# Kernel tuning notes

Hardware: AMD Instinct MI355X
Metric: run time of the kernel (lower is better)

## Reference

```python
import jax, jax.numpy as jnp
from jax import lax
import numpy as np

N_NODES = 512
BATCH = 256
N_STEPS = 200
DT = 0.02  # t_span spacing; keeps 200 RK4 steps numerically tame


def setup_inputs() -> dict:
    key = jax.random.key(0)
    ks = jax.random.split(key, 7)
    s = 1.0 / np.sqrt(N_NODES)
    x_init = jax.random.normal(ks[0], (BATCH, N_NODES), dtype=jnp.float32)
    t_span = jnp.arange(N_STEPS, dtype=jnp.float32) * DT
    # MaskedLinear params (kaiming-uniform-ish scale)
    W1 = jax.random.uniform(ks[1], (N_NODES, N_NODES), jnp.float32, -s, s)
    b1 = jax.random.uniform(ks[2], (N_NODES,), jnp.float32, -s, s)
    # inner Linear params
    W2 = jax.random.uniform(ks[3], (N_NODES, N_NODES), jnp.float32, -s, s)
    b2 = jax.random.uniform(ks[4], (N_NODES,), jnp.float32, -s, s)
    mask = jax.random.bernoulli(ks[5], 0.1, (N_NODES, N_NODES)).astype(jnp.float32)
    mask = mask * (1.0 - jnp.eye(N_NODES, dtype=jnp.float32))
    return {"x_init": x_init, "t_span": t_span, "W1": W1, "b1": b1,
            "W2": W2, "b2": b2, "mask": mask}


def reference(x_init, t_span, W1, b1, W2, b2, mask):
    # ODE func: dydt = W2 @ tanh(masked(W1) @ y + b1) + b2 (t unused)
    Wm = W1 * mask  # [N, N]
    def f(y):  # y: [B, N]
        return jnp.tanh(y @ Wm.T + b1) @ W2.T + b2

    dts = t_span[1:] - t_span[:-1]  # [T-1]

    def rk4_step(y, dt):
        k1 = f(y)
        k2 = f(y + dt * k1 / 2)
        k3 = f(y + dt * k2 / 2)
        k4 = f(y + dt * k3)
        y_new = y + dt / 6 * (k1 + 2 * k2 + 2 * k3 + k4)
        return y_new, y_new

    _, traj = lax.scan(rk4_step, x_init, dts)  # [T-1, B, N]
    traj = jnp.concatenate([x_init[None], traj], axis=0)  # [T, B, N]
    return jnp.transpose(traj, (1, 0, 2))  # [B, T, N]
```

## Files before the change

kernel.cpp:

```cpp
#include <hip/hip_runtime.h>
#include <math.h>

#define NN 512
#define NB 256
#define NT 200
#define TPB 256
#define NTEAM 8

typedef unsigned long long u64;
typedef _Float16 half8 __attribute__((ext_vector_type(8)));
typedef float f32x4 __attribute__((ext_vector_type(4)));

#define WS_WM  0
#define WS_WC  (NN*NN)
#define WS_C   (WS_WC + NN*NN/2)
#define WS_H   (WS_C + NN)
#define WS_CNT (WS_H + NB*NN)

__device__ __forceinline__ void sysst_u64(u64* p, u64 v) {
  __hip_atomic_store(p, v, __ATOMIC_RELAXED, __HIP_MEMORY_SCOPE_SYSTEM);
}
__device__ __forceinline__ u64 sysld_u64(const u64* p) {
  return __hip_atomic_load(p, __ATOMIC_RELAXED, __HIP_MEMORY_SCOPE_SYSTEM);
}
__device__ __forceinline__ void sysst_f1(float* p, float v) {
  __hip_atomic_store(p, v, __ATOMIC_RELAXED, __HIP_MEMORY_SCOPE_SYSTEM);
}
__device__ __forceinline__ float sysld_f1(const float* p) {
  return __hip_atomic_load(p, __ATOMIC_RELAXED, __HIP_MEMORY_SCOPE_SYSTEM);
}

__global__ __launch_bounds__(256)
void k_init(const float* __restrict__ W1, const float* __restrict__ mask,
            const float* __restrict__ x_init, float* __restrict__ ws,
            float* __restrict__ out) {
  int gt = blockIdx.x * 256 + threadIdx.x;
  int stride = gridDim.x * 256;
  for (int i = gt; i < NN * NN; i += stride) ws[WS_WM + i] = W1[i] * mask[i];
  for (int i = gt; i < NB * NN / 2; i += stride) {
    u64 q = ((const u64*)x_init)[i];
    int r = i >> 8, np = i & 255;
    *((u64*)(out + (size_t)r * NT * NN) + np) = q;
  }
  if (gt < 32 * NTEAM * 16)
    __hip_atomic_store(((unsigned*)(ws + WS_CNT)) + gt, 0u,
                       __ATOMIC_RELAXED, __HIP_MEMORY_SCOPE_SYSTEM);
}

__global__ __launch_bounds__(128)
void k_prep(const float* __restrict__ W2g, const float* __restrict__ b2,
            const float* __restrict__ x_init, float* __restrict__ ws) {
  __shared__ float w1row[NN];
  const int j = blockIdx.x;
  const int t = threadIdx.x;
  const float* wm = ws + WS_WM + (size_t)j * NN;
  for (int i = t; i < NN; i += 128) w1row[i] = wm[i];
  __syncthreads();

  f32x4 acc = {0.f, 0.f, 0.f, 0.f};
  for (int m = 0; m < NN; ++m) {
    float w = w1row[m];
    if (w != 0.f)
      acc += w * ((const f32x4*)(W2g + (size_t)m * NN))[t];
  }
  _Float16* wcrow = (_Float16*)(ws + WS_WC) + (size_t)j * NN;
#pragma unroll
  for (int e = 0; e < 4; ++e) wcrow[4 * t + e] = (_Float16)acc[e];

  if (t == 0) {
    float s = 0.f;
    for (int m = 0; m < NN; ++m)
      if (w1row[m] != 0.f) s += b2[m] * w1row[m];
    ws[WS_C + j] = s;
  }

#pragma unroll
  for (int rr = 0; rr < 2; ++rr) {
    int r = t + rr * 128;
    const float* y0 = x_init + (size_t)r * NN;
    float s = 0.f;
    for (int m = 0; m < NN; ++m) {
      float w = w1row[m];
      if (w != 0.f) s = fmaf(y0[m], w, s);
    }
    sysst_f1(ws + WS_H + (size_t)r * NN + j, s);
  }
}

__device__ __forceinline__ void team_release(unsigned* flags, int cg, unsigned e) {
  __syncthreads();
  if (threadIdx.x == 0)
    __hip_atomic_store(flags + cg * 16, e, __ATOMIC_RELAXED,
                       __HIP_MEMORY_SCOPE_SYSTEM);
}
__device__ __forceinline__ void team_wait(unsigned* flags, unsigned e) {
  if (threadIdx.x < NTEAM) {
    while (__hip_atomic_load(flags + threadIdx.x * 16, __ATOMIC_RELAXED,
                             __HIP_MEMORY_SCOPE_AGENT) < e)
      __builtin_amdgcn_s_sleep(1);
  }
  __syncthreads();
}

__device__ __forceinline__ void stage8(_Float16* __restrict__ pH,
                                       _Float16* __restrict__ pL,
                                       const float* __restrict__ src,
                                       int tid) {
  const int row = tid >> 5;
  const int segq = tid & 31;
  const u64* s = (const u64*)(src + (size_t)row * NN) + segq * 8;
  u64 tmp[8];
#pragma unroll
  for (int i = 0; i < 8; ++i) tmp[i] = sysld_u64(s + i);
  half8* dH = (half8*)pH;
  half8* dL = (half8*)pL;
#pragma unroll
  for (int q = 0; q < 2; ++q) {
    half8 hv, lv;
#pragma unroll
    for (int e = 0; e < 4; ++e) {
      union { u64 q64; float f[2]; } u; u.q64 = tmp[q * 4 + e];
#pragma unroll
      for (int x = 0; x < 2; ++x) {
        float f = u.f[x]; _Float16 h = (_Float16)f;
        hv[e * 2 + x] = h;
        lv[e * 2 + x] = (_Float16)((f - (float)h) * 2048.0f);
      }
    }
    int g = segq * 2 + q;
    int idx = row * 64 + (g ^ row);
    dH[idx] = hv; dL[idx] = lv;
  }
}

__device__ __forceinline__ void gemm_tile(const _Float16* yHb, const _Float16* yLb,
                                          const _Float16* wb,
                                          int rc, int kg, int wv, float res[4]) {
  const int swz = rc & 7;
  const half8* pAH = (const half8*)yHb;
  const half8* pAL = (const half8*)yLb;
  const half8* pB  = (const half8*)wb;
  const int abase = (rc & 7) * 64;
  const int bbase = (wv * 16 + rc) * 64;
  f32x4 aH = {0.f, 0.f, 0.f, 0.f};
  f32x4 aL = {0.f, 0.f, 0.f, 0.f};
#pragma unroll
  for (int kt = 0; kt < 16; ++kt) {
    const int gs = (kt * 4 + kg) ^ swz;
    half8 av = pAH[abase + gs];
    half8 al = pAL[abase + gs];
    half8 bv = pB[bbase + gs];
    aH = __builtin_amdgcn_mfma_f32_16x16x32_f16(av, bv, aH, 0, 0, 0);
    aL = __builtin_amdgcn_mfma_f32_16x16x32_f16(al, bv, aL, 0, 0, 0);
  }
#pragma unroll
  for (int r = 0; r < 4; ++r) res[r] = aH[r] + aL[r] * (1.0f / 2048.0f);
}

__global__ __launch_bounds__(TPB, 1)
void k_ode(const float* __restrict__ tspan,
           const float* __restrict__ W2g,
           const float* __restrict__ b1,
           const float* __restrict__ b2,
           float* __restrict__ ws,
           float* __restrict__ out,
           const float* __restrict__ x_init) {
  extern __shared__ _Float16 ldsh[];
  _Float16* wc = ldsh;
  _Float16* w2 = ldsh + 32768;
  _Float16* hH = ldsh + 65536;
  _Float16* hL = ldsh + 73728;

  const int bid = blockIdx.x;
  const int cg = bid & 7, rg = bid >> 3;
  const int r0 = rg * 8, j0 = cg * 64;
  const int tid = threadIdx.x;
  const int lane = tid & 63, wv = tid >> 6;
  const int rc = lane & 15, kg = lane >> 4;
  const int mycol = j0 + wv * 16 + rc;
  const bool act = (kg < 2);

  float* hbuf = ws + WS_H;
  unsigned* flags = ((unsigned*)(ws + WS_CNT)) + rg * (NTEAM * 16);

  {
    const int col = tid >> 2;
    const int part = tid & 3;
    const half8* s1 = (const half8*)((const _Float16*)(ws + WS_WC)
                                     + (size_t)(j0 + col) * NN) + part * 16;
    const float* s2 = W2g + (size_t)(j0 + col) * NN + part * 128;
    half8* d1 = (half8*)wc;
    half8* d2 = (half8*)w2;
    const int key = col & 7;
#pragma unroll
    for (int i = 0; i < 16; ++i) {
      int g = part * 16 + i;
      int idx = col * 64 + (g ^ key);
      d1[idx] = s1[i];
      half8 hv;
#pragma unroll
      for (int e = 0; e < 8; ++e) hv[e] = (_Float16)s2[i * 8 + e];
      d2[idx] = hv;
    }
  }
  const float b1s = b1[mycol], b2s = b2[mycol];
  const float c_own = ws[WS_C + mycol];

  float xb[4], yb[4];
  if (act) {
#pragma unroll
    for (int r = 0; r < 4; ++r) {
      xb[r] = sysld_f1(hbuf + (size_t)(r0 + kg * 4 + r) * NN + mycol);
      yb[r] = x_init[(size_t)(r0 + kg * 4 + r) * NN + mycol];
    }
  }
  __syncthreads();

  unsigned epoch = 0;
  float res[4], res2[4];

  for (int t = 0; t < NT - 1; ++t) {
    const float dt = tspan[t + 1] - tspan[t];
    const float alf[3] = {dt * 0.5f, dt * 0.5f, dt};
    float xs[4], H[4];
    if (act) {
#pragma unroll
      for (int r = 0; r < 4; ++r) xs[r] = xb[r];
    }
#pragma unroll
    for (int s = 0; s < 3; ++s) {
      if (act) {
#pragma unroll
        for (int r = 0; r < 4; ++r) {
          float h = tanhf(xs[r] + b1s);
          H[r] = (s == 0) ? h : fmaf(2.f, h, H[r]);
          sysst_f1(hbuf + (size_t)(r0 + kg * 4 + r) * NN + mycol, h);
        }
      }
      team_release(flags, cg, ++epoch);
      team_wait(flags, epoch);
      stage8(hH, hL, hbuf + (size_t)r0 * NN, tid);
      __syncthreads();
      gemm_tile(hH, hL, wc, rc, kg, wv, res);
      if (act) {
#pragma unroll
        for (int r = 0; r < 4; ++r)
          xs[r] = xb[r] + alf[s] * (res[r] + c_own);
      }
    }
    if (act) {
#pragma unroll
      for (int r = 0; r < 4; ++r) {
        H[r] += tanhf(xs[r] + b1s);
        sysst_f1(hbuf + (size_t)(r0 + kg * 4 + r) * NN + mycol, H[r]);
      }
    }
    team_release(flags, cg, ++epoch);
    team_wait(flags, epoch);
    stage8(hH, hL, hbuf + (size_t)r0 * NN, tid);
    __syncthreads();
    gemm_tile(hH, hL, wc, rc, kg, wv, res);
    gemm_tile(hH, hL, w2, rc, kg, wv, res2);
    if (act) {
      const float c6 = dt / 6.0f;
#pragma unroll
      for (int r = 0; r < 4; ++r) {
        xb[r] += c6 * res[r] + dt * c_own;
        yb[r] += c6 * res2[r] + dt * b2s;
        out[((size_t)(r0 + kg * 4 + r) * NT + (t + 1)) * NN + mycol] = yb[r];
      }
    }
  }
}

extern "C" void kernel_launch(void* const* d_in, const int* in_sizes, int n_in,
                              void* d_out, int out_size, void* d_ws, size_t ws_size,
                              hipStream_t stream) {
  const float* x_init = (const float*)d_in[0];
  const float* tspan  = (const float*)d_in[1];
  const float* W1     = (const float*)d_in[2];
  const float* b1     = (const float*)d_in[3];
  const float* W2     = (const float*)d_in[4];
  const float* b2     = (const float*)d_in[5];
  const float* mask   = (const float*)d_in[6];
  float* out = (float*)d_out;
  float* ws  = (float*)d_ws;

  hipLaunchKernelGGL(k_init, dim3(256), dim3(256), 0, stream,
                     W1, mask, x_init, ws, out);
  hipLaunchKernelGGL(k_prep, dim3(512), dim3(128), 0, stream,
                     W2, b2, x_init, ws);

  const unsigned ldsBytes = 160 * 1024;
  (void)hipFuncSetAttribute((const void*)k_ode,
                            hipFuncAttributeMaxDynamicSharedMemorySize,
                            (int)ldsBytes);

  hipLaunchKernelGGL(k_ode, dim3(256), dim3(TPB), ldsBytes, stream,
                     tspan, W2, b1, b2, ws, out, x_init);
}
```

Before: 2.895 ms.

## Split team sync into two half-row groups with double-buffered hidden state

Result: slower. 3.666 ms (+26.6%).

```diff
diff --git a/kernel.cpp b/kernel.cpp
--- a/kernel.cpp
+++ b/kernel.cpp
@@ -42,7 +42,7 @@
     int r = i >> 8, np = i & 255;
     *((u64*)(out + (size_t)r * NT * NN) + np) = q;
   }
-  if (gt < 32 * NTEAM * 16)
+  if (gt < 32 * 2 * NTEAM * 16)
     __hip_atomic_store(((unsigned*)(ws + WS_CNT)) + gt, 0u,
                        __ATOMIC_RELAXED, __HIP_MEMORY_SCOPE_SYSTEM);
 }
@@ -87,50 +87,46 @@
   }
 }
 
-__device__ __forceinline__ void team_release(unsigned* flags, int cg, unsigned e) {
+__device__ __forceinline__ void team_wait(unsigned* flagsp, unsigned target) {
+  if (threadIdx.x < NTEAM) {
+    while (__hip_atomic_load(flagsp + threadIdx.x * 16, __ATOMIC_RELAXED,
+                             __HIP_MEMORY_SCOPE_AGENT) < target)
+      __builtin_amdgcn_s_sleep(1);
+  }
+  __syncthreads();
+}
+__device__ __forceinline__ void team_release(unsigned* flagsp, int cg, unsigned e) {
   __syncthreads();
   if (threadIdx.x == 0)
-    __hip_atomic_store(flags + cg * 16, e, __ATOMIC_RELAXED,
+    __hip_atomic_store(flagsp + cg * 16, e, __ATOMIC_RELAXED,
                        __HIP_MEMORY_SCOPE_SYSTEM);
 }
-__device__ __forceinline__ void team_wait(unsigned* flags, unsigned e) {
-  if (threadIdx.x < NTEAM) {
-    while (__hip_atomic_load(flags + threadIdx.x * 16, __ATOMIC_RELAXED,
-                             __HIP_MEMORY_SCOPE_AGENT) < e)
-      __builtin_amdgcn_s_sleep(1);
-  }
-  __syncthreads();
-}
-
-__device__ __forceinline__ void stage8(_Float16* __restrict__ pH,
+
+__device__ __forceinline__ void stage4(_Float16* __restrict__ pH,
                                        _Float16* __restrict__ pL,
                                        const float* __restrict__ src,
-                                       int tid) {
-  const int row = tid >> 5;
-  const int segq = tid & 31;
-  const u64* s = (const u64*)(src + (size_t)row * NN) + segq * 8;
-  u64 tmp[8];
-#pragma unroll
-  for (int i = 0; i < 8; ++i) tmp[i] = sysld_u64(s + i);
-  half8* dH = (half8*)pH;
-  half8* dL = (half8*)pL;
-#pragma unroll
-  for (int q = 0; q < 2; ++q) {
-    half8 hv, lv;
-#pragma unroll
-    for (int e = 0; e < 4; ++e) {
-      union { u64 q64; float f[2]; } u; u.q64 = tmp[q * 4 + e];
-#pragma unroll
-      for (int x = 0; x < 2; ++x) {
-        float f = u.f[x]; _Float16 h = (_Float16)f;
-        hv[e * 2 + x] = h;
-        lv[e * 2 + x] = (_Float16)((f - (float)h) * 2048.0f);
-      }
-    }
-    int g = segq * 2 + q;
-    int idx = row * 64 + (g ^ row);
-    dH[idx] = hv; dL[idx] = lv;
-  }
+                                       int p, int tid) {
+  const int row = tid >> 6;
+  const int g = tid & 63;
+  const u64* s = (const u64*)(src + (size_t)row * NN) + g * 4;
+  u64 tmp[4];
+#pragma unroll
+  for (int i = 0; i < 4; ++i) tmp[i] = sysld_u64(s + i);
+  half8 hv, lv;
+#pragma unroll
+  for (int e = 0; e < 4; ++e) {
+    union { u64 q64; float f[2]; } u; u.q64 = tmp[e];
+#pragma unroll
+    for (int x = 0; x < 2; ++x) {
+      float f = u.f[x]; _Float16 h = (_Float16)f;
+      hv[e * 2 + x] = h;
+      lv[e * 2 + x] = (_Float16)((f - (float)h) * 2048.0f);
+    }
+  }
+  const int dr = p * 4 + row;
+  const int idx = dr * 64 + (g ^ dr);
+  ((half8*)pH)[idx] = hv;
+  ((half8*)pL)[idx] = lv;
 }
 
 __device__ __forceinline__ void gemm_tile(const _Float16* yHb, const _Float16* yLb,
@@ -169,7 +165,7 @@
   _Float16* wc = ldsh;
   _Float16* w2 = ldsh + 32768;
   _Float16* hH = ldsh + 65536;
-  _Float16* hL = ldsh + 73728;
+  _Float16* hL = ldsh + 69632;
 
   const int bid = blockIdx.x;
   const int cg = bid & 7, rg = bid >> 3;
@@ -180,8 +176,11 @@
   const int mycol = j0 + wv * 16 + rc;
   const bool act = (kg < 2);
 
-  float* hbuf = ws + WS_H;
-  unsigned* flags = ((unsigned*)(ws + WS_CNT)) + rg * (NTEAM * 16);
+  float* hb[2];
+  hb[0] = ws + WS_H;
+  hb[1] = ws + WS_WM;
+  unsigned* flagsA = ((unsigned*)(ws + WS_CNT)) + rg * (2 * NTEAM * 16);
+  unsigned* flagsB = flagsA + NTEAM * 16;
 
   {
     const int col = tid >> 2;
@@ -206,68 +205,68 @@
   const float b1s = b1[mycol], b2s = b2[mycol];
   const float c_own = ws[WS_C + mycol];
 
-  float xb[4], yb[4];
+  float xb[4], yb[4], H[4];
   if (act) {
 #pragma unroll
     for (int r = 0; r < 4; ++r) {
-      xb[r] = sysld_f1(hbuf + (size_t)(r0 + kg * 4 + r) * NN + mycol);
+      xb[r] = sysld_f1(hb[0] + (size_t)(r0 + kg * 4 + r) * NN + mycol);
       yb[r] = x_init[(size_t)(r0 + kg * 4 + r) * NN + mycol];
+      H[r] = tanhf(xb[r] + b1s);
+      sysst_f1(hb[0] + (size_t)(r0 + kg * 4 + r) * NN + mycol, H[r]);
     }
   }
   __syncthreads();
-
-  unsigned epoch = 0;
+  if (tid == 0) {
+    __hip_atomic_store(flagsA + cg * 16, 1u, __ATOMIC_RELAXED,
+                       __HIP_MEMORY_SCOPE_SYSTEM);
+    __hip_atomic_store(flagsB + cg * 16, 1u, __ATOMIC_RELAXED,
+                       __HIP_MEMORY_SCOPE_SYSTEM);
+  }
+
   float res[4], res2[4];
 
   for (int t = 0; t < NT - 1; ++t) {
     const float dt = tspan[t + 1] - tspan[t];
-    const float alf[3] = {dt * 0.5f, dt * 0.5f, dt};
-    float xs[4], H[4];
-    if (act) {
-#pragma unroll
-      for (int r = 0; r < 4; ++r) xs[r] = xb[r];
-    }
-#pragma unroll
-    for (int s = 0; s < 3; ++s) {
-      if (act) {
-#pragma unroll
-        for (int r = 0; r < 4; ++r) {
-          float h = tanhf(xs[r] + b1s);
-          H[r] = (s == 0) ? h : fmaf(2.f, h, H[r]);
-          sysst_f1(hbuf + (size_t)(r0 + kg * 4 + r) * NN + mycol, h);
+    const float c6 = dt / 6.0f;
+#pragma unroll 1
+    for (int s = 0; s < 4; ++s) {
+      const int q = t * 4 + s;
+      const unsigned target = (unsigned)(q + 1);
+      const float* rdb = hb[q & 1];
+      float* wrb = hb[(q + 1) & 1];
+#pragma unroll
+      for (int p = 0; p < 2; ++p) {
+        unsigned* fl = p ? flagsB : flagsA;
+        team_wait(fl, target);
+        stage4(hH, hL, rdb + (size_t)(r0 + p * 4) * NN, p, tid);
+        __syncthreads();
+        gemm_tile(hH, hL, wc, rc, kg, wv, res);
+        if (s == 3) gemm_tile(hH, hL, w2, rc, kg, wv, res2);
+        if (kg == p) {
+          if (s < 3) {
+            const float a = (s == 2) ? dt : dt * 0.5f;
+#pragma unroll
+            for (int r = 0; r < 4; ++r) {
+              float xs = xb[r] + a * (res[r] + c_own);
+              float h = tanhf(xs + b1s);
+              float st;
+              if (s == 2) { H[r] += h;       st = H[r]; }
+              else        { H[r] += 2.f * h; st = h;    }
+              sysst_f1(wrb + (size_t)(r0 + p * 4 + r) * NN + mycol, st);
+            }
+          } else {
+#pragma unroll
+            for (int r = 0; r < 4; ++r) {
+              xb[r] += c6 * res[r] + dt * c_own;
+              yb[r] += c6 * res2[r] + dt * b2s;
+              out[((size_t)(r0 + p * 4 + r) * NT + (t + 1)) * NN + mycol] = yb[r];
+              float h = tanhf(xb[r] + b1s);
+              H[r] = h;
+              sysst_f1(wrb + (size_t)(r0 + p * 4 + r) * NN + mycol, h);
+            }
+          }
         }
-      }
-      team_release(flags, cg, ++epoch);
-      team_wait(flags, epoch);
-      stage8(hH, hL, hbuf + (size_t)r0 * NN, tid);
-      __syncthreads();
-      gemm_tile(hH, hL, wc, rc, kg, wv, res);
-      if (act) {
-#pragma unroll
-        for (int r = 0; r < 4; ++r)
-          xs[r] = xb[r] + alf[s] * (res[r] + c_own);
-      }
-    }
-    if (act) {
-#pragma unroll
-      for (int r = 0; r < 4; ++r) {
-        H[r] += tanhf(xs[r] + b1s);
-        sysst_f1(hbuf + (size_t)(r0 + kg * 4 + r) * NN + mycol, H[r]);
-      }
-    }
-    team_release(flags, cg, ++epoch);
-    team_wait(flags, epoch);
-    stage8(hH, hL, hbuf + (size_t)r0 * NN, tid);
-    __syncthreads();
-    gemm_tile(hH, hL, wc, rc, kg, wv, res);
-    gemm_tile(hH, hL, w2, rc, kg, wv, res2);
-    if (act) {
-      const float c6 = dt / 6.0f;
-#pragma unroll
-      for (int r = 0; r < 4; ++r) {
-        xb[r] += c6 * res[r] + dt * c_own;
-        yb[r] += c6 * res2[r] + dt * b2s;
-        out[((size_t)(r0 + kg * 4 + r) * NT + (t + 1)) * NN + mycol] = yb[r];
+        team_release(fl, cg, target + 1);
       }
     }
   }
@@ -291,7 +290,7 @@
   hipLaunchKernelGGL(k_prep, dim3(512), dim3(128), 0, stream,
                      W2, b2, x_init, ws);
 
-  const unsigned ldsBytes = 160 * 1024;
+  const unsigned ldsBytes = 144 * 1024;
   (void)hipFuncSetAttribute((const void*)k_ode,
                             hipFuncAttributeMaxDynamicSharedMemorySize,
                             (int)ldsBytes);
```
